# Kernel optimization log

Hardware: AMD Instinct MI355X
Metric: run time of the kernel (lower is better)

## Reference

```python
import jax, jax.numpy as jnp
import numpy as np

B, N, DIN, DH, DOUT = 4096, 16, 256, 256, 256  # batch rows, num_variables, per-var dims


def _ln(x, g, b, eps=1e-5):
    m = jnp.mean(x, axis=-1, keepdims=True)
    v = jnp.var(x, axis=-1, keepdims=True)
    return (x - m) * jax.lax.rsqrt(v + eps) * g + b


def setup_inputs() -> dict:
    key = jax.random.key(0)
    ks = jax.random.split(key, 10)
    s = 0.02
    f32 = jnp.float32
    return {
        "x": jax.random.normal(ks[0], (B, N, DIN), f32),
        # per-variable GRN params, stacked along variable axis (batched GEMMs)
        "vW2": s * jax.random.normal(ks[1], (N, DIN, DH), f32),
        "vb2": jnp.zeros((N, DH), f32),
        "vW1": s * jax.random.normal(ks[2], (N, DH, DOUT), f32),
        "vb1": jnp.zeros((N, DOUT), f32),
        "vW4": s * jax.random.normal(ks[3], (N, DOUT, DOUT), f32),
        "vb4": jnp.zeros((N, DOUT), f32),
        "vW5": s * jax.random.normal(ks[4], (N, DOUT, DOUT), f32),
        "vb5": jnp.zeros((N, DOUT), f32),
        "vlng": jnp.ones((N, DOUT), f32),
        "vlnb": jnp.zeros((N, DOUT), f32),
        # concat GRN params (operate on flattened n*in features)
        "cW2": s * jax.random.normal(ks[5], (N * DIN, N * DH), f32),
        "cb2": jnp.zeros((N * DH,), f32),
        "cW1": s * jax.random.normal(ks[6], (N * DH, N * DOUT), f32),
        "cb1": jnp.zeros((N * DOUT,), f32),
        "cW4": s * jax.random.normal(ks[7], (N * DOUT, N * DOUT), f32),
        "cb4": jnp.zeros((N * DOUT,), f32),
        "cW5": s * jax.random.normal(ks[8], (N * DOUT, N * DOUT), f32),
        "cb5": jnp.zeros((N * DOUT,), f32),
        "clng": jnp.ones((N * DOUT,), f32),
        "clnb": jnp.zeros((N * DOUT,), f32),
    }


def reference(x, vW2, vb2, vW1, vb1, vW4, vb4, vW5, vb5, vlng, vlnb,
              cW2, cb2, cW1, cb1, cW4, cb4, cW5, cb5, clng, clnb):
    b = x.shape[0]
    flat = x.reshape(b, N * DIN)                       # torch.cat(inputs) over feature dim
    # ---- concat GRN: ELU dense -> dense -> GLU -> residual layernorm ----
    h = jax.nn.elu(flat @ cW2 + cb2)                   # [b, N*DH]
    e1 = h @ cW1 + cb1                                 # [b, N*DOUT]
    g = jax.nn.sigmoid(e1 @ cW4 + cb4) * (e1 @ cW5 + cb5)
    c = _ln(flat + g, clng, clnb)                      # [b, N*DOUT] (in==out, identity skip)
    # ---- softmax selection weights over the variable axis ----
    w = jax.nn.softmax(c.reshape(b, N, DOUT), axis=1)  # [b, N, DOUT]
    # ---- per-variable GRNs as batched GEMMs over the variable axis ----
    hv = jax.nn.elu(jnp.einsum('bni,nih->bnh', x, vW2) + vb2)
    e1v = jnp.einsum('bnh,nho->bno', hv, vW1) + vb1
    gv = (jax.nn.sigmoid(jnp.einsum('bno,nop->bnp', e1v, vW4) + vb4)
          * (jnp.einsum('bno,nop->bnp', e1v, vW5) + vb5))
    yv = _ln(x + gv, vlng, vlnb)                       # [b, N, DOUT]
    # ---- weighted combine (v^T @ x in the original) ----
    return jnp.sum(w * yv, axis=1)                     # [b, DOUT]
```

## Files before the change

kernel.cpp:

```cpp
#include <hip/hip_runtime.h>
#include <hip/hip_bf16.h>
#include <math.h>
#include <type_traits>

typedef __hip_bfloat16 bf16;
typedef __attribute__((ext_vector_type(8))) short short8;
typedef __attribute__((ext_vector_type(4))) float f32x4;

#define DEV __device__ __forceinline__

template<int V> using IC = std::integral_constant<int, V>;

DEV void gload_lds16(const bf16* g, bf16* l) {
    __builtin_amdgcn_global_load_lds(
        (const __attribute__((address_space(1))) void*)(g),
        (__attribute__((address_space(3))) void*)(l), 16, 0, 0);
}

#define VMW(n) do { asm volatile("s_waitcnt vmcnt(" #n ")" ::: "memory"); \
                    __builtin_amdgcn_sched_barrier(0); } while (0)

template<int ACT>
__global__ __launch_bounds__(512, 2)
void gemm256_k(const bf16* __restrict__ Am, int lda, long aBatch,
               const bf16* __restrict__ Bm, int ldb, long bBatch,
               const float* __restrict__ biasp, long biasBatch,
               bf16* __restrict__ Cm, int ldc, long cBatch, int K)
{
    extern __shared__ char lds[];
    const int bz = blockIdx.z;
    const bf16* A = Am + (long)bz * aBatch;
    const bf16* B = Bm + (long)bz * bBatch;
    const float* bias = biasp + (long)bz * biasBatch;
    bf16* C = Cm + (long)bz * cBatch;

    const int nwg = gridDim.x * gridDim.y;
    int flat = blockIdx.y * gridDim.x + blockIdx.x;
    if ((nwg & 7) == 0 && nwg >= 8) flat = (flat & 7) * (nwg >> 3) + (flat >> 3);
    const int bx = flat % gridDim.x, by = flat / gridDim.x;
    const int rowBase = by * 256, colBase = bx * 256;

    const int tid = threadIdx.x;
    const int wid = tid >> 6, lane = tid & 63;
    const int wr = wid >> 2, wc = wid & 3;
    const int lr = lane & 15, lg = lane >> 4;

    const int r     = (tid >> 2) & 15;
    const int cbyte = (tid & 3) * 16;
    const int c0    = ((r & 8) ? (cbyte ^ 32) : cbyte) >> 1;
    const int srow  = (wid >> 1) * 16 + r;
    const int scol  = (wid & 1) * 32 + c0;

    const bf16* Ap = A + (long)(rowBase + srow) * lda + scol;
    const bf16* Bp = B + (long)(colBase + srow) * ldb + scol;

    const int cb  = (lr & 8) ? ((lg * 16) ^ 32) : (lg * 16);
    const int aRd = wr * 8192 + lr * 64 + cb;
    const int bRd = wc * 4096 + lr * 64 + cb;

    f32x4  acc[2][2][4][2] = {};
    short8 aF[2][4][2];
    short8 bF[2][2][2];

    const int T = K >> 6;

    auto stageA = [&](int tt, int h) {
        bf16* d = (bf16*)(lds + (tt & 1) * 32768 + h * 16384 + wid * 1024);
        const bf16* s = Ap + tt * 64 + (long)h * 128 * lda;
        gload_lds16(s, d);
        gload_lds16(s + (long)64 * lda, (bf16*)((char*)d + 8192));
    };
    auto stageB = [&](int tt, int h) {
        bf16* d = (bf16*)(lds + 65536 + (tt & 1) * 32768 + h * 16384 + wid * 1024);
        const bf16* s = Bp + tt * 64 + (long)h * 128 * ldb;
        gload_lds16(s, d);
        gload_lds16(s + (long)64 * ldb, (bf16*)((char*)d + 8192));
    };
    auto readA = [&](int tt, auto qmc) {
        constexpr int qm = decltype(qmc)::value;
        const char* base = lds + (tt & 1) * 32768 + qm * 16384 + aRd;
        #pragma unroll
        for (int mi = 0; mi < 4; mi++)
            #pragma unroll
            for (int ks = 0; ks < 2; ks++)
                aF[qm][mi][ks] = *(const short8*)(base + mi * 2048 + ks * 1024);
    };
    auto readB = [&](int tt, auto qnc) {
        constexpr int qn = decltype(qnc)::value;
        const char* base = lds + 65536 + (tt & 1) * 32768 + qn * 16384 + bRd;
        #pragma unroll
        for (int ni = 0; ni < 2; ni++)
            #pragma unroll
            for (int ks = 0; ks < 2; ks++)
                bF[qn][ni][ks] = *(const short8*)(base + ni * 2048 + ks * 1024);
    };
    auto mma = [&](auto qmc, auto qnc) {
        constexpr int qm = decltype(qmc)::value;
        constexpr int qn = decltype(qnc)::value;
        __builtin_amdgcn_s_setprio(1);
        #pragma unroll
        for (int mi = 0; mi < 4; mi++)
          #pragma unroll
          for (int ni = 0; ni < 2; ni++)
            #pragma unroll
            for (int ks = 0; ks < 2; ks++)
              acc[qm][qn][mi][ni] = __builtin_amdgcn_mfma_f32_16x16x32_bf16(
                  aF[qm][mi][ks], bF[qn][ni][ks], acc[qm][qn][mi][ni], 0, 0, 0);
        __builtin_amdgcn_s_setprio(0);
    };
    auto bar = [&]() {
        __builtin_amdgcn_sched_barrier(0);
        __builtin_amdgcn_s_barrier();
        __builtin_amdgcn_sched_barrier(0);
    };

    stageA(0, 0); stageB(0, 0); stageA(0, 1); stageB(0, 1);
    if (T > 1) stageA(1, 0);
    VMW(6);
    bar();
    readA(0, IC<0>{}); readB(0, IC<0>{});

    for (int t = 0; t < T; t++) {
        const bool last  = (t == T - 1);
        const bool last2 = (t == T - 2);
        if (!last) stageB(t + 1, 0);
        if (!last) { VMW(6); } else { VMW(2); }
        bar();
        readA(t, IC<1>{});
        mma(IC<0>{}, IC<0>{});
        bar();
        if (!last) stageA(t + 1, 1);
        if (!last) { VMW(6); } else { VMW(0); }
        bar();
        readB(t, IC<1>{});
        mma(IC<1>{}, IC<0>{});
        bar();
        if (!last) stageB(t + 1, 1);
        bar();
        mma(IC<1>{}, IC<1>{});
        bar();
        if (t + 2 < T) stageA(t + 2, 0);
        if (!last) { if (last2) { VMW(4); } else { VMW(6); } }
        bar();
        mma(IC<0>{}, IC<1>{});
        if (!last) { readA(t + 1, IC<0>{}); readB(t + 1, IC<0>{}); }
        bar();
    }

    const long ldcL = ldc;
    #pragma unroll
    for (int qm = 0; qm < 2; qm++)
      #pragma unroll
      for (int mi = 0; mi < 4; mi++) {
        const int row0 = rowBase + qm * 128 + wr * 64 + mi * 16 + lg * 4;
        #pragma unroll
        for (int qn = 0; qn < 2; qn++)
          #pragma unroll
          for (int ni = 0; ni < 2; ni++) {
            const int col = colBase + qn * 128 + wc * 32 + ni * 16 + lr;
            const float bv = bias[col];
            #pragma unroll
            for (int i = 0; i < 4; i++) {
                float v = acc[qm][qn][mi][ni][i] + bv;
                if (ACT == 1) v = v > 0.f ? v : expm1f(v);
                C[(long)(row0 + i) * ldcL + col] = __float2bfloat16(v);
            }
          }
      }
}

__global__ __launch_bounds__(256)
void cvt_k(const float* __restrict__ in, bf16* __restrict__ out)
{
    const long i = ((long)blockIdx.x * 256 + threadIdx.x) * 8;
    float4 u = *(const float4*)(in + i);
    float4 v = *(const float4*)(in + i + 4);
    bf16 t[8];
    t[0] = __float2bfloat16(u.x); t[1] = __float2bfloat16(u.y);
    t[2] = __float2bfloat16(u.z); t[3] = __float2bfloat16(u.w);
    t[4] = __float2bfloat16(v.x); t[5] = __float2bfloat16(v.y);
    t[6] = __float2bfloat16(v.z); t[7] = __float2bfloat16(v.w);
    *(short8*)(out + i) = *(short8*)t;
}

struct TPtrs { const float* s[4]; bf16* d[4]; };

__global__ __launch_bounds__(256)
void transpose_cvt_k(TPtrs p, int R, int nsub)
{
    const int z = blockIdx.z;
    const int widx = z / nsub, sub = z - widx * nsub;
    const float* __restrict__ in = p.s[widx] + (long)sub * R * R;
    bf16* __restrict__ outp = p.d[widx] + (long)sub * R * R;

    __shared__ float tile[32][33];
    const int c0 = blockIdx.x * 32, r0 = blockIdx.y * 32;
    const int tx = threadIdx.x & 31, ty = threadIdx.x >> 5;
    #pragma unroll
    for (int i = 0; i < 4; i++)
        tile[ty + i * 8][tx] = in[(long)(r0 + ty + i * 8) * R + c0 + tx];
    __syncthreads();
    #pragma unroll
    for (int i = 0; i < 4; i++)
        outp[(long)(c0 + ty + i * 8) * R + r0 + tx] = __float2bfloat16(tile[tx][ty + i * 8]);
}

DEV float2 block_reduce2_bcast(float a, float b, float* ldsr)
{
    const int lane = threadIdx.x & 63, wid = threadIdx.x >> 6;
    #pragma unroll
    for (int off = 32; off > 0; off >>= 1) {
        a += __shfl_down(a, off, 64);
        b += __shfl_down(b, off, 64);
    }
    __syncthreads();
    if (lane == 0) { ldsr[wid] = a; ldsr[wid + 4] = b; }
    __syncthreads();
    float2 rr;
    rr.x = ldsr[0] + ldsr[1] + ldsr[2] + ldsr[3];
    rr.y = ldsr[4] + ldsr[5] + ldsr[6] + ldsr[7];
    return rr;
}

__global__ __launch_bounds__(256)
void ln_softmax_k(const float* __restrict__ x,
                  const bf16* __restrict__ e4, const bf16* __restrict__ e5,
                  const float* __restrict__ gamma, const float* __restrict__ beta,
                  bf16* __restrict__ w)
{
    const int b = blockIdx.x, d = threadIdx.x;
    const long base = (long)b * 4096;
    __shared__ float red[8];

    float s[16];
    float sum = 0.f, sumsq = 0.f;
    #pragma unroll
    for (int n = 0; n < 16; n++) {
        const long idx = base + n * 256 + d;
        float g4 = __bfloat162float(e4[idx]);
        float g5 = __bfloat162float(e5[idx]);
        float v = x[idx] + g5 / (1.f + expf(-g4));
        s[n] = v; sum += v; sumsq += v * v;
    }
    float2 t = block_reduce2_bcast(sum, sumsq, red);
    const float mean = t.x * (1.f / 4096.f);
    const float var  = t.y * (1.f / 4096.f) - mean * mean;
    const float rstd = rsqrtf(var + 1e-5f);

    float mx = -1e30f;
    #pragma unroll
    for (int n = 0; n < 16; n++) {
        float c = (s[n] - mean) * rstd * gamma[n * 256 + d] + beta[n * 256 + d];
        s[n] = c; mx = fmaxf(mx, c);
    }
    float denom = 0.f;
    #pragma unroll
    for (int n = 0; n < 16; n++) { float e = expf(s[n] - mx); s[n] = e; denom += e; }
    const float rden = 1.f / denom;
    #pragma unroll
    for (int n = 0; n < 16; n++)
        w[base + n * 256 + d] = __float2bfloat16(s[n] * rden);
}

__global__ __launch_bounds__(256)
void combine_k(const float* __restrict__ x,
               const bf16* __restrict__ e4v, const bf16* __restrict__ e5v,
               const bf16* __restrict__ w,
               const float* __restrict__ vlng, const float* __restrict__ vlnb,
               float* __restrict__ out)
{
    const int b = blockIdx.x, d = threadIdx.x;
    const long base = (long)b * 4096;
    __shared__ float red[8];
    float acc = 0.f;
    for (int n = 0; n < 16; n++) {
        const long idx = base + n * 256 + d;
        float g4 = __bfloat162float(e4v[idx]);
        float g5 = __bfloat162float(e5v[idx]);
        float v = x[idx] + g5 / (1.f + expf(-g4));
        float2 t = block_reduce2_bcast(v, v * v, red);
        const float mean = t.x * (1.f / 256.f);
        const float var  = t.y * (1.f / 256.f) - mean * mean;
        const float yv = (v - mean) * rsqrtf(var + 1e-5f) * vlng[n * 256 + d] + vlnb[n * 256 + d];
        acc += __bfloat162float(w[idx]) * yv;
    }
    out[(long)b * 256 + d] = acc;
}

extern "C" void kernel_launch(void* const* d_in, const int* in_sizes, int n_in,
                              void* d_out, int out_size, void* d_ws, size_t ws_size,
                              hipStream_t stream)
{
    const float* x    = (const float*)d_in[0];
    const float* vW2  = (const float*)d_in[1];
    const float* vb2  = (const float*)d_in[2];
    const float* vW1  = (const float*)d_in[3];
    const float* vb1  = (const float*)d_in[4];
    const float* vW4  = (const float*)d_in[5];
    const float* vb4  = (const float*)d_in[6];
    const float* vW5  = (const float*)d_in[7];
    const float* vb5  = (const float*)d_in[8];
    const float* vlng = (const float*)d_in[9];
    const float* vlnb = (const float*)d_in[10];
    const float* cW2  = (const float*)d_in[11];
    const float* cb2  = (const float*)d_in[12];
    const float* cW1  = (const float*)d_in[13];
    const float* cb1  = (const float*)d_in[14];
    const float* cW4  = (const float*)d_in[15];
    const float* cb4  = (const float*)d_in[16];
    const float* cW5  = (const float*)d_in[17];
    const float* cb5  = (const float*)d_in[18];
    const float* clng = (const float*)d_in[19];
    const float* clnb = (const float*)d_in[20];
    float* out = (float*)d_out;
    (void)n_in; (void)out_size; (void)ws_size;

    const int NB = in_sizes[0] / 4096;
    const long XF = (long)NB * 4096;

    char* ws = (char*)d_ws;
    size_t off = 0;
    auto alloc = [&](size_t bytes) {
        char* p = ws + off;
        off += (bytes + 255) & ~(size_t)255;
        return p;
    };
    bf16* xb   = (bf16*)alloc(XF * 2);
    bf16* cW2t = (bf16*)alloc(4096L * 4096 * 2);
    bf16* cW1t = (bf16*)alloc(4096L * 4096 * 2);
    bf16* cW4t = (bf16*)alloc(4096L * 4096 * 2);
    bf16* cW5t = (bf16*)alloc(4096L * 4096 * 2);
    bf16* vW2t = (bf16*)alloc(16L * 256 * 256 * 2);
    bf16* vW1t = (bf16*)alloc(16L * 256 * 256 * 2);
    bf16* vW4t = (bf16*)alloc(16L * 256 * 256 * 2);
    bf16* vW5t = (bf16*)alloc(16L * 256 * 256 * 2);
    bf16* bufA = (bf16*)alloc(XF * 2);
    bf16* bufB = (bf16*)alloc(XF * 2);
    bf16* bufW = (bf16*)alloc(XF * 2);
    bf16* bufC = cW1t;
    bf16* bufD = cW2t;

    hipFuncSetAttribute(reinterpret_cast<const void*>(gemm256_k<0>),
                        hipFuncAttributeMaxDynamicSharedMemorySize, 131072);
    hipFuncSetAttribute(reinterpret_cast<const void*>(gemm256_k<1>),
                        hipFuncAttributeMaxDynamicSharedMemorySize, 131072);

    const int MB = NB / 256;

    cvt_k<<<dim3((unsigned)(XF / 2048)), 256, 0, stream>>>(x, xb);

    TPtrs pb;
    pb.s[0] = cW2; pb.s[1] = cW1; pb.s[2] = cW4; pb.s[3] = cW5;
    pb.d[0] = cW2t; pb.d[1] = cW1t; pb.d[2] = cW4t; pb.d[3] = cW5t;
    transpose_cvt_k<<<dim3(128, 128, 4), 256, 0, stream>>>(pb, 4096, 1);

    TPtrs pv;
    pv.s[0] = vW2; pv.s[1] = vW1; pv.s[2] = vW4; pv.s[3] = vW5;
    pv.d[0] = vW2t; pv.d[1] = vW1t; pv.d[2] = vW4t; pv.d[3] = vW5t;
    transpose_cvt_k<<<dim3(8, 8, 64), 256, 0, stream>>>(pv, 256, 16);

    gemm256_k<1><<<dim3(16, MB, 1), 512, 131072, stream>>>(
        xb, 4096, 0, cW2t, 4096, 0, cb2, 0, bufA, 4096, 0, 4096);
    gemm256_k<0><<<dim3(16, MB, 1), 512, 131072, stream>>>(
        bufA, 4096, 0, cW1t, 4096, 0, cb1, 0, bufB, 4096, 0, 4096);
    gemm256_k<0><<<dim3(16, MB, 1), 512, 131072, stream>>>(
        bufB, 4096, 0, cW4t, 4096, 0, cb4, 0, bufC, 4096, 0, 4096);
    gemm256_k<0><<<dim3(16, MB, 1), 512, 131072, stream>>>(
        bufB, 4096, 0, cW5t, 4096, 0, cb5, 0, bufD, 4096, 0, 4096);
    ln_softmax_k<<<dim3(NB), 256, 0, stream>>>(x, bufC, bufD, clng, clnb, bufW);

    gemm256_k<1><<<dim3(1, MB, 16), 512, 131072, stream>>>(
        xb, 4096, 256, vW2t, 256, 65536, vb2, 256, bufA, 4096, 256, 256);
    gemm256_k<0><<<dim3(1, MB, 16), 512, 131072, stream>>>(
        bufA, 4096, 256, vW1t, 256, 65536, vb1, 256, bufB, 4096, 256, 256);
    gemm256_k<0><<<dim3(1, MB, 16), 512, 131072, stream>>>(
        bufB, 4096, 256, vW4t, 256, 65536, vb4, 256, bufC, 4096, 256, 256);
    gemm256_k<0><<<dim3(1, MB, 16), 512, 131072, stream>>>(
        bufB, 4096, 256, vW5t, 256, 65536, vb5, 256, bufD, 4096, 256, 256);

    combine_k<<<dim3(NB), 256, 0, stream>>>(x, bufC, bufD, bufW, vlng, vlnb, out);
}
```

Measured before the change: 1.069 ms.

## Deepen GEMM prefetch to two K-tiles and fuse softmax with combine kernel

Result: faster. 997.0 us (-6.7%).

```diff
diff --git a/kernel.cpp b/kernel.cpp
--- a/kernel.cpp
+++ b/kernel.cpp
@@ -18,6 +18,8 @@
 }
 
 #define VMW(n) do { asm volatile("s_waitcnt vmcnt(" #n ")" ::: "memory"); \
+                    __builtin_amdgcn_sched_barrier(0); } while (0)
+#define LKW0() do { asm volatile("s_waitcnt lgkmcnt(0)" ::: "memory"); \
                     __builtin_amdgcn_sched_barrier(0); } while (0)
 
 template<int ACT>
@@ -115,35 +117,26 @@
     };
 
     stageA(0, 0); stageB(0, 0); stageA(0, 1); stageB(0, 1);
-    if (T > 1) stageA(1, 0);
-    VMW(6);
+    if (T > 1) { stageA(1, 0); stageB(1, 0); stageA(1, 1); stageB(1, 1); VMW(8); }
+    else       { VMW(0); }
     bar();
-    readA(0, IC<0>{}); readB(0, IC<0>{});
+    readA(0, IC<0>{});
 
     for (int t = 0; t < T; t++) {
-        const bool last  = (t == T - 1);
-        const bool last2 = (t == T - 2);
-        if (!last) stageB(t + 1, 0);
-        if (!last) { VMW(6); } else { VMW(2); }
-        bar();
+        const bool s2 = (t + 2 < T);
+        readB(t, IC<0>{});
+        if (s2) stageA(t + 2, 0);
+        bar(); mma(IC<0>{}, IC<0>{}); bar();
         readA(t, IC<1>{});
-        mma(IC<0>{}, IC<0>{});
-        bar();
-        if (!last) stageA(t + 1, 1);
-        if (!last) { VMW(6); } else { VMW(0); }
-        bar();
+        if (s2) stageB(t + 2, 0);
+        bar(); mma(IC<1>{}, IC<0>{}); bar();
         readB(t, IC<1>{});
-        mma(IC<1>{}, IC<0>{});
-        bar();
-        if (!last) stageB(t + 1, 1);
-        bar();
-        mma(IC<1>{}, IC<1>{});
-        bar();
-        if (t + 2 < T) stageA(t + 2, 0);
-        if (!last) { if (last2) { VMW(4); } else { VMW(6); } }
-        bar();
-        mma(IC<0>{}, IC<1>{});
-        if (!last) { readA(t + 1, IC<0>{}); readB(t + 1, IC<0>{}); }
+        if (s2) stageA(t + 2, 1);
+        bar(); mma(IC<1>{}, IC<1>{}); bar();
+        if (s2)               { stageB(t + 2, 1); VMW(8); }
+        else if (t + 2 == T)  { VMW(0); }
+        bar(); mma(IC<0>{}, IC<1>{});
+        if (t + 1 < T) { readA(t + 1, IC<0>{}); LKW0(); }
         bar();
     }
 
@@ -222,24 +215,28 @@
     return rr;
 }
 
+DEV float glu(float g4, float g5) { return g5 / (1.f + expf(-g4)); }
+
 __global__ __launch_bounds__(256)
-void ln_softmax_k(const float* __restrict__ x,
-                  const bf16* __restrict__ e4, const bf16* __restrict__ e5,
-                  const float* __restrict__ gamma, const float* __restrict__ beta,
-                  bf16* __restrict__ w)
+void final_k(const float* __restrict__ x,
+             const bf16* __restrict__ e4, const bf16* __restrict__ e5,
+             const bf16* __restrict__ e4v, const bf16* __restrict__ e5v,
+             const float* __restrict__ clng, const float* __restrict__ clnb,
+             const float* __restrict__ vlng, const float* __restrict__ vlnb,
+             float* __restrict__ out)
 {
     const int b = blockIdx.x, d = threadIdx.x;
     const long base = (long)b * 4096;
     __shared__ float red[8];
 
-    float s[16];
+    float xv[16], s[16];
     float sum = 0.f, sumsq = 0.f;
     #pragma unroll
     for (int n = 0; n < 16; n++) {
         const long idx = base + n * 256 + d;
-        float g4 = __bfloat162float(e4[idx]);
-        float g5 = __bfloat162float(e5[idx]);
-        float v = x[idx] + g5 / (1.f + expf(-g4));
+        float xx = x[idx];
+        xv[n] = xx;
+        float v = xx + glu(__bfloat162float(e4[idx]), __bfloat162float(e5[idx]));
         s[n] = v; sum += v; sumsq += v * v;
     }
     float2 t = block_reduce2_bcast(sum, sumsq, red);
@@ -250,39 +247,23 @@
     float mx = -1e30f;
     #pragma unroll
     for (int n = 0; n < 16; n++) {
-        float c = (s[n] - mean) * rstd * gamma[n * 256 + d] + beta[n * 256 + d];
+        float c = (s[n] - mean) * rstd * clng[n * 256 + d] + clnb[n * 256 + d];
         s[n] = c; mx = fmaxf(mx, c);
     }
     float denom = 0.f;
     #pragma unroll
     for (int n = 0; n < 16; n++) { float e = expf(s[n] - mx); s[n] = e; denom += e; }
     const float rden = 1.f / denom;
-    #pragma unroll
-    for (int n = 0; n < 16; n++)
-        w[base + n * 256 + d] = __float2bfloat16(s[n] * rden);
-}
-
-__global__ __launch_bounds__(256)
-void combine_k(const float* __restrict__ x,
-               const bf16* __restrict__ e4v, const bf16* __restrict__ e5v,
-               const bf16* __restrict__ w,
-               const float* __restrict__ vlng, const float* __restrict__ vlnb,
-               float* __restrict__ out)
-{
-    const int b = blockIdx.x, d = threadIdx.x;
-    const long base = (long)b * 4096;
-    __shared__ float red[8];
+
     float acc = 0.f;
     for (int n = 0; n < 16; n++) {
         const long idx = base + n * 256 + d;
-        float g4 = __bfloat162float(e4v[idx]);
-        float g5 = __bfloat162float(e5v[idx]);
-        float v = x[idx] + g5 / (1.f + expf(-g4));
-        float2 t = block_reduce2_bcast(v, v * v, red);
-        const float mean = t.x * (1.f / 256.f);
-        const float var  = t.y * (1.f / 256.f) - mean * mean;
-        const float yv = (v - mean) * rsqrtf(var + 1e-5f) * vlng[n * 256 + d] + vlnb[n * 256 + d];
-        acc += __bfloat162float(w[idx]) * yv;
+        float v = xv[n] + glu(__bfloat162float(e4v[idx]), __bfloat162float(e5v[idx]));
+        float2 tt = block_reduce2_bcast(v, v * v, red);
+        const float m2 = tt.x * (1.f / 256.f);
+        const float v2 = tt.y * (1.f / 256.f) - m2 * m2;
+        const float yv = (v - m2) * rsqrtf(v2 + 1e-5f) * vlng[n * 256 + d] + vlnb[n * 256 + d];
+        acc += s[n] * rden * yv;
     }
     out[(long)b * 256 + d] = acc;
 }
@@ -336,9 +317,10 @@
     bf16* vW5t = (bf16*)alloc(16L * 256 * 256 * 2);
     bf16* bufA = (bf16*)alloc(XF * 2);
     bf16* bufB = (bf16*)alloc(XF * 2);
-    bf16* bufW = (bf16*)alloc(XF * 2);
-    bf16* bufC = cW1t;
-    bf16* bufD = cW2t;
+    bf16* e4  = cW2t;
+    bf16* e5  = cW1t;
+    bf16* e4v = cW4t;
+    bf16* e5v = cW5t;
 
     hipFuncSetAttribute(reinterpret_cast<const void*>(gemm256_k<0>),
                         hipFuncAttributeMaxDynamicSharedMemorySize, 131072);
@@ -364,19 +346,19 @@
     gemm256_k<0><<<dim3(16, MB, 1), 512, 131072, stream>>>(
         bufA, 4096, 0, cW1t, 4096, 0, cb1, 0, bufB, 4096, 0, 4096);
     gemm256_k<0><<<dim3(16, MB, 1), 512, 131072, stream>>>(
-        bufB, 4096, 0, cW4t, 4096, 0, cb4, 0, bufC, 4096, 0, 4096);
+        bufB, 4096, 0, cW4t, 4096, 0, cb4, 0, e4, 4096, 0, 4096);
     gemm256_k<0><<<dim3(16, MB, 1), 512, 131072, stream>>>(
-        bufB, 4096, 0, cW5t, 4096, 0, cb5, 0, bufD, 4096, 0, 4096);
-    ln_softmax_k<<<dim3(NB), 256, 0, stream>>>(x, bufC, bufD, clng, clnb, bufW);
+        bufB, 4096, 0, cW5t, 4096, 0, cb5, 0, e5, 4096, 0, 4096);
 
     gemm256_k<1><<<dim3(1, MB, 16), 512, 131072, stream>>>(
         xb, 4096, 256, vW2t, 256, 65536, vb2, 256, bufA, 4096, 256, 256);
     gemm256_k<0><<<dim3(1, MB, 16), 512, 131072, stream>>>(
         bufA, 4096, 256, vW1t, 256, 65536, vb1, 256, bufB, 4096, 256, 256);
     gemm256_k<0><<<dim3(1, MB, 16), 512, 131072, stream>>>(
-        bufB, 4096, 256, vW4t, 256, 65536, vb4, 256, bufC, 4096, 256, 256);
+        bufB, 4096, 256, vW4t, 256, 65536, vb4, 256, e4v, 4096, 256, 256);
     gemm256_k<0><<<dim3(1, MB, 16), 512, 131072, stream>>>(
-        bufB, 4096, 256, vW5t, 256, 65536, vb5, 256, bufD, 4096, 256, 256);
-
-    combine_k<<<dim3(NB), 256, 0, stream>>>(x, bufC, bufD, bufW, vlng, vlnb, out);
-}
+        bufB, 4096, 256, vW5t, 256, 65536, vb5, 256, e5v, 4096, 256, 256);
+
+    final_k<<<dim3(NB), 256, 0, stream>>>(
+        x, e4, e5, e4v, e5v, clng, clnb, vlng, vlnb, out);
+}
```
